# Optimization experiments

Hardware: AMD Instinct MI355X
Metric: run time of the kernel (lower is better)

## Reference

```python
import jax, jax.numpy as jnp
import numpy as np

B, S = 8, 1024                      # num sequences, per-seq prefill length (uniform ragged batch)
NUM_HEADS, HEAD_DIM, NUM_KV_HEADS = 32, 128, 8
GROUP = NUM_HEADS // NUM_KV_HEADS   # GQA repeat factor
SCALE = 1.0 / float(np.sqrt(HEAD_DIM))
T = B * S                           # total tokens in batch
NUM_SLOTS = 16384                   # KV-cache slots
DKV = NUM_KV_HEADS * HEAD_DIM


def setup_inputs() -> dict:
    key = jax.random.key(0)
    ks = jax.random.split(key, 4)
    q = jax.random.normal(ks[0], (T, NUM_HEADS * HEAD_DIM), dtype=jnp.float32)
    k = jax.random.normal(ks[1], (T, DKV), dtype=jnp.float32)
    v = jax.random.normal(ks[2], (T, DKV), dtype=jnp.float32)
    k_cache = jnp.zeros((NUM_SLOTS, DKV), dtype=jnp.float32)
    v_cache = jnp.zeros((NUM_SLOTS, DKV), dtype=jnp.float32)
    # distinct slots per token (pure prefill: gather mapping == store mapping)
    slot_mapping = jax.random.permutation(ks[3], NUM_SLOTS)[:T].astype(jnp.int32)
    seq_slot_mapping = slot_mapping
    return {"q": q, "k": k, "v": v, "k_cache": k_cache, "v_cache": v_cache,
            "slot_mapping": slot_mapping, "seq_slot_mapping": seq_slot_mapping}


def reference(q, k, v, k_cache, v_cache, slot_mapping, seq_slot_mapping):
    # reshape to per-head layout
    kr = k.reshape(T, DKV)
    vr = v.reshape(T, DKV)
    # store_kvcache: scatter new k/v into paged cache by slot
    k_cache = k_cache.at[slot_mapping].set(kr)
    v_cache = v_cache.at[slot_mapping].set(vr)
    # get_kvcache: gather the per-sequence contiguous KV from the cache
    ck = k_cache[seq_slot_mapping].reshape(B, S, NUM_KV_HEADS, HEAD_DIM)
    cv = v_cache[seq_slot_mapping].reshape(B, S, NUM_KV_HEADS, HEAD_DIM)
    qb = q.reshape(B, S, NUM_HEADS, HEAD_DIM)
    # GQA: repeat_interleave kv heads (matches torch SDPA enable_gqa)
    ck = jnp.repeat(ck, GROUP, axis=2)  # [B,S,H,D]
    cv = jnp.repeat(cv, GROUP, axis=2)
    scores = jnp.einsum("bqhd,bkhd->bhqk", qb, ck) * SCALE  # [B,H,S,S]
    causal = jnp.tril(jnp.ones((S, S), dtype=bool))
    scores = jnp.where(causal[None, None], scores, jnp.finfo(scores.dtype).min)
    probs = jax.nn.softmax(scores, axis=-1)
    o = jnp.einsum("bhqk,bkhd->bqhd", probs, cv)  # [B,S,H,D]
    return o.reshape(T, NUM_HEADS * HEAD_DIM)
```

## Files before the change

### kernel.cpp

```cpp
#include <hip/hip_runtime.h>

#define NB 8
#define NS 1024
#define NH 32
#define NKV 8
#define ND 128
#define QT 256
#define KT 64

typedef _Float16 f16x8 __attribute__((ext_vector_type(8)));
typedef __fp16 fp16x2 __attribute__((ext_vector_type(2)));
typedef float f32x16 __attribute__((ext_vector_type(16)));
typedef unsigned int u32x2 __attribute__((ext_vector_type(2)));

__device__ __forceinline__ float exp2fast(float x) { return __builtin_amdgcn_exp2f(x); }
__device__ __forceinline__ unsigned pkrtz_u(float a, float b) {
  union { fp16x2 h; unsigned u; } c;
  c.h = __builtin_amdgcn_cvt_pkrtz(a, b);
  return c.u;
}
__device__ __forceinline__ u32x2 swap32(float x) {
  union { float f; unsigned u; } c; c.f = x;
  return __builtin_amdgcn_permlane32_swap(c.u, c.u, false, false);
}
__device__ __forceinline__ float asf(unsigned u) { union { unsigned u; float f; } c; c.u = u; return c.f; }

__global__ __launch_bounds__(256)
void cvt_kf(const float* __restrict__ kg, char* __restrict__ wsK)
{
  int g = blockIdx.x * 256 + threadIdx.x;
  int t = g >> 7, c8 = g & 127;
  int hkv = c8 >> 4, d8 = c8 & 15;
  const float* src = kg + (size_t)t * 1024 + hkv * 128 + d8 * 8;
  float4 a = *(const float4*)src;
  float4 c = *(const float4*)(src + 4);
  f16x8 h8;
  h8[0] = (_Float16)a.x; h8[1] = (_Float16)a.y; h8[2] = (_Float16)a.z; h8[3] = (_Float16)a.w;
  h8[4] = (_Float16)c.x; h8[5] = (_Float16)c.y; h8[6] = (_Float16)c.z; h8[7] = (_Float16)c.w;
  int b  = t >> 10, kv = t & 1023;
  int ti = kv >> 6, kvl = kv & 63, kb = kvl >> 5, lq = kvl & 31;
  int dblk = d8 >> 1, hi = d8 & 1;
  size_t off = (((size_t)(b * 8 + hkv) * 16 + ti) * 16 + kb * 8 + dblk) * 1024 + (hi * 32 + lq) * 16;
  *(f16x8*)(wsK + off) = h8;
}

__global__ __launch_bounds__(256)
void cvt_vf(const float* __restrict__ vg, _Float16* __restrict__ wsV)
{
  __shared__ _Float16 T[ND][KT];
  const int tid = threadIdx.x;
  const int kvt = blockIdx.x, b = blockIdx.y, hkv = blockIdx.z;
#pragma unroll
  for (int pass = 0; pass < 8; ++pass) {
    int kvr = (tid >> 5) + pass * 8;
    int d4  = (tid & 31) * 4;
    float4 v = ((const float4*)vg)[(size_t)(b * NS + kvt * KT + kvr) * 256 + hkv * 32 + (tid & 31)];
    T[d4 + 0][kvr] = (_Float16)v.x;
    T[d4 + 1][kvr] = (_Float16)v.y;
    T[d4 + 2][kvr] = (_Float16)v.z;
    T[d4 + 3][kvr] = (_Float16)v.w;
  }
  __syncthreads();
  _Float16* out = wsV + ((size_t)(b * 8 + hkv) * 16 + kvt) * 8192;
#pragma unroll
  for (int pass = 0; pass < 4; ++pass) {
    int unit = tid + pass * 256;
    int c = unit >> 6, lane = unit & 63;
    int d = (c & 3) * 32 + (lane & 31);
    int kv8 = (c >> 2) * 16 + (lane >> 5) * 8;
    *(f16x8*)(out + unit * 8) = *(const f16x8*)&T[d][kv8];
  }
}

__global__ __launch_bounds__(512, 1)
void attn_fwd(const float* __restrict__ qg, const char* __restrict__ wsK,
              const char* __restrict__ wsV, float* __restrict__ og)
{
  __shared__ __align__(16) char Klds[2][16384];
  __shared__ __align__(16) char Vlds[2][16384];

  const int id = blockIdx.x;
  const int v  = (id & 7) * 32 + (id >> 3);
  const int panel = v >> 2;
  const int sub   = v & 3;
  const int b     = panel >> 3;
  const int hkv   = panel & 7;
  const int h     = hkv * 4 + sub;

  const int tid  = threadIdx.x;
  const int lane = tid & 63;
  const int w    = tid >> 6;
  const int lq   = lane & 31;
  const int hi   = lane >> 5;

  const float QS = 0.08838834764831845f * 1.4426950408889634f;

  const char* wsKb = wsK + (size_t)panel * 16 * 16384;
  const char* wsVb = wsV + (size_t)panel * 16 * 16384;

  const int o0 = tid * 16;
  const int o1 = (tid + 512) * 16;

  f16x8 kpre0, kpre1, vpre0, vpre1;

  const int qorder[4] = {0, 3, 1, 2};

#pragma unroll 1
  for (int ph = 0; ph < 4; ++ph) {
    const int qtile = qorder[ph];
    const int wv    = (ph & 1) ? (7 - w) : w;
    const int qr0w  = qtile * QT + wv * 32;
    const int qrow  = qr0w + lq;

    f16x8 qf[8];
    {
      const float* qp = qg + (size_t)(b * NS + qrow) * (NH * ND) + h * ND + hi * 8;
#pragma unroll
      for (int dblk = 0; dblk < 8; ++dblk) {
        float4 f0 = *(const float4*)(qp + dblk * 16);
        float4 f1 = *(const float4*)(qp + dblk * 16 + 4);
        f16x8 a;
        a[0] = (_Float16)(f0.x * QS); a[1] = (_Float16)(f0.y * QS);
        a[2] = (_Float16)(f0.z * QS); a[3] = (_Float16)(f0.w * QS);
        a[4] = (_Float16)(f1.x * QS); a[5] = (_Float16)(f1.y * QS);
        a[6] = (_Float16)(f1.z * QS); a[7] = (_Float16)(f1.w * QS);
        qf[dblk] = a;
      }
    }

    f32x16 acc[4];
#pragma unroll
    for (int nb = 0; nb < 4; ++nb)
#pragma unroll
      for (int r = 0; r < 16; ++r) acc[nb][r] = 0.f;
    float m_run = -1e30f, l_run = 0.f;

    const int nt = (qtile + 1) * (QT / KT);

    {
      kpre0 = *(const f16x8*)(wsKb + o0); kpre1 = *(const f16x8*)(wsKb + o1);
      vpre0 = *(const f16x8*)(wsVb + o0); vpre1 = *(const f16x8*)(wsVb + o1);
      *(f16x8*)(&Klds[0][0] + o0) = kpre0; *(f16x8*)(&Klds[0][0] + o1) = kpre1;
      *(f16x8*)(&Vlds[0][0] + o0) = vpre0; *(f16x8*)(&Vlds[0][0] + o1) = vpre1;
    }
    asm volatile("s_waitcnt lgkmcnt(0)" ::: "memory");
    __builtin_amdgcn_s_barrier();
    __builtin_amdgcn_sched_barrier(0);

#pragma unroll 1
    for (int ti = 0; ti < nt; ++ti) {
      const int kv0 = ti * KT;
      const int cur = ti & 1;
      const bool hn = (ti + 1 < nt);

      if (hn) {
        const char* gk = wsKb + (size_t)(ti + 1) * 16384;
        const char* gv = wsVb + (size_t)(ti + 1) * 16384;
        kpre0 = *(const f16x8*)(gk + o0); kpre1 = *(const f16x8*)(gk + o1);
        vpre0 = *(const f16x8*)(gv + o0); vpre1 = *(const f16x8*)(gv + o1);
      }

      const bool live = (kv0 <= qr0w + 31);
      f16x8 pa[4];
      if (live) {
        const char* Kb = &Klds[cur][0];

        f32x16 s[2];
#pragma unroll
        for (int r = 0; r < 16; ++r) { s[0][r] = 0.f; s[1][r] = 0.f; }
        __builtin_amdgcn_s_setprio(1);
#pragma unroll
        for (int dblk = 0; dblk < 8; ++dblk) {
          f16x8 k0 = *(const f16x8*)(Kb + dblk * 1024 + lane * 16);
          f16x8 k1 = *(const f16x8*)(Kb + (8 + dblk) * 1024 + lane * 16);
          s[0] = __builtin_amdgcn_mfma_f32_32x32x16_f16(k0, qf[dblk], s[0], 0, 0, 0);
          s[1] = __builtin_amdgcn_mfma_f32_32x32x16_f16(k1, qf[dblk], s[1], 0, 0, 0);
        }
        __builtin_amdgcn_s_setprio(0);

        if (kv0 + KT - 1 > qr0w) {
          const int thr = qrow - kv0;
#pragma unroll
          for (int kb = 0; kb < 2; ++kb)
#pragma unroll
            for (int r = 0; r < 16; ++r) {
              int kvl = kb * 32 + (r & 3) + 8 * (r >> 2) + 4 * hi;
              if (kvl > thr) s[kb][r] = -1e30f;
            }
        }

        float pmax = s[0][0];
#pragma unroll
        for (int r = 1; r < 16; ++r) pmax = fmaxf(pmax, s[0][r]);
#pragma unroll
        for (int r = 0; r < 16; ++r) pmax = fmaxf(pmax, s[1][r]);
        {
          u32x2 pr = swap32(pmax);
          pmax = fmaxf(asf(pr[0]), asf(pr[1]));
        }
        const int need = !__all(pmax <= m_run + 8.0f);
        if (need) {
          const float mn = fmaxf(m_run, pmax);
          const float al = exp2fast(m_run - mn);
          m_run = mn;
#pragma unroll
          for (int r = 0; r < 16; ++r) {
            int row = (r & 3) + 8 * (r >> 2) + 4 * hi;
            float a = __shfl(al, row, 64);
#pragma unroll
            for (int nb = 0; nb < 4; ++nb) acc[nb][r] *= a;
          }
          l_run *= al;
        }
        float rs = 0.f;
#pragma unroll
        for (int kb = 0; kb < 2; ++kb)
#pragma unroll
          for (int r = 0; r < 16; ++r) {
            float pv = exp2fast(s[kb][r] - m_run);
            s[kb][r] = pv;
            rs += pv;
          }
        {
          u32x2 sr = swap32(rs);
          rs = asf(sr[0]) + asf(sr[1]);
        }
        l_run += rs;

#pragma unroll
        for (int t = 0; t < 4; ++t) {
          const int kb = t >> 1, rb = (t & 1) * 8;
          unsigned w0 = pkrtz_u(s[kb][rb + 0], s[kb][rb + 1]);
          unsigned w1 = pkrtz_u(s[kb][rb + 2], s[kb][rb + 3]);
          unsigned w2 = pkrtz_u(s[kb][rb + 4], s[kb][rb + 5]);
          unsigned w3 = pkrtz_u(s[kb][rb + 6], s[kb][rb + 7]);
          u32x2 p02 = __builtin_amdgcn_permlane32_swap(w0, w2, false, false);
          u32x2 p13 = __builtin_amdgcn_permlane32_swap(w1, w3, false, false);
          union { unsigned u[4]; f16x8 v; } pw;
          pw.u[0] = p02[0]; pw.u[1] = p13[0]; pw.u[2] = p02[1]; pw.u[3] = p13[1];
          pa[t] = pw.v;
        }
      }

      if (hn) {
        *(f16x8*)(&Klds[cur ^ 1][0] + o0) = kpre0;
        *(f16x8*)(&Klds[cur ^ 1][0] + o1) = kpre1;
        *(f16x8*)(&Vlds[cur ^ 1][0] + o0) = vpre0;
        *(f16x8*)(&Vlds[cur ^ 1][0] + o1) = vpre1;
      }

      if (live) {
        const char* Vb = &Vlds[cur][0];
        __builtin_amdgcn_s_setprio(1);
#pragma unroll
        for (int t = 0; t < 4; ++t)
#pragma unroll
          for (int nb = 0; nb < 4; ++nb) {
            f16x8 vb = *(const f16x8*)(Vb + (t * 4 + nb) * 1024 + lane * 16);
            acc[nb] = __builtin_amdgcn_mfma_f32_32x32x16_f16(pa[t], vb, acc[nb], 0, 0, 0);
          }
        __builtin_amdgcn_s_setprio(0);
      }

      asm volatile("s_waitcnt lgkmcnt(0)" ::: "memory");
      __builtin_amdgcn_s_barrier();
      __builtin_amdgcn_sched_barrier(0);
    }

    const float linv = 1.0f / l_run;
#pragma unroll
    for (int r = 0; r < 16; ++r) {
      int row = (r & 3) + 8 * (r >> 2) + 4 * hi;
      float li = __shfl(linv, row, 64);
      float* op = og + (size_t)(b * NS + qr0w + row) * (NH * ND) + h * ND + lq;
#pragma unroll
      for (int nb = 0; nb < 4; ++nb)
        op[nb * 32] = acc[nb][r] * li;
    }
    __builtin_amdgcn_s_barrier();
  }
}

extern "C" void kernel_launch(void* const* d_in, const int* in_sizes, int n_in,
                              void* d_out, int out_size, void* d_ws, size_t ws_size,
                              hipStream_t stream) {
  const float* q = (const float*)d_in[0];
  const float* k = (const float*)d_in[1];
  const float* v = (const float*)d_in[2];
  float* o = (float*)d_out;

  const size_t KSZ = (size_t)NB * NKV * NS * ND * sizeof(_Float16);
  if (ws_size < 2 * KSZ) return;
  char*     wsK = (char*)d_ws;
  _Float16* wsV = (_Float16*)((char*)d_ws + KSZ);

  cvt_kf<<<dim3((NB * NS * 128) / 256), 256, 0, stream>>>(k, wsK);
  cvt_vf<<<dim3(NS / KT, NB, NKV),      256, 0, stream>>>(v, wsV);
  attn_fwd<<<dim3(256),                 512, 0, stream>>>(q, wsK, (const char*)wsV, o);
}
```

Baseline: 162.0 us.

## Process KV tiles in pairs with 4-stage LDS ring and staggered wave order

Expands the K/V LDS buffers from double to quad buffering and processes two KV tiles per loop iteration with a single barrier, halving barrier count. Odd and even waves process the two tiles in swapped order to desynchronize LDS reads and MFMA/softmax phases across waves. Global prefetch for the next pair is interleaved between the two tile computations. This costs twice the LDS footprint and more register pressure for the inlined lambda bodies.

```diff
diff --git a/kernel.cpp b/kernel.cpp
--- a/kernel.cpp
+++ b/kernel.cpp
@@ -76,8 +76,8 @@
 void attn_fwd(const float* __restrict__ qg, const char* __restrict__ wsK,
               const char* __restrict__ wsV, float* __restrict__ og)
 {
-  __shared__ __align__(16) char Klds[2][16384];
-  __shared__ __align__(16) char Vlds[2][16384];
+  __shared__ __align__(16) char Klds[4][16384];
+  __shared__ __align__(16) char Vlds[4][16384];
 
   const int id = blockIdx.x;
   const int v  = (id & 7) * 32 + (id >> 3);
@@ -135,131 +135,148 @@
       for (int r = 0; r < 16; ++r) acc[nb][r] = 0.f;
     float m_run = -1e30f, l_run = 0.f;
 
-    const int nt = (qtile + 1) * (QT / KT);
-
-    {
-      kpre0 = *(const f16x8*)(wsKb + o0); kpre1 = *(const f16x8*)(wsKb + o1);
-      vpre0 = *(const f16x8*)(wsVb + o0); vpre1 = *(const f16x8*)(wsVb + o1);
-      *(f16x8*)(&Klds[0][0] + o0) = kpre0; *(f16x8*)(&Klds[0][0] + o1) = kpre1;
-      *(f16x8*)(&Vlds[0][0] + o0) = vpre0; *(f16x8*)(&Vlds[0][0] + o1) = vpre1;
-    }
+    auto compute_tile = [&](int t) {
+      const int kv0 = t * KT;
+      if (kv0 > qr0w + 31) return;
+      const char* Kb = &Klds[t & 3][0];
+      const char* Vb = &Vlds[t & 3][0];
+
+      f32x16 s[2];
+#pragma unroll
+      for (int r = 0; r < 16; ++r) { s[0][r] = 0.f; s[1][r] = 0.f; }
+      __builtin_amdgcn_s_setprio(1);
+#pragma unroll
+      for (int dblk = 0; dblk < 8; ++dblk) {
+        f16x8 k0 = *(const f16x8*)(Kb + dblk * 1024 + lane * 16);
+        f16x8 k1 = *(const f16x8*)(Kb + (8 + dblk) * 1024 + lane * 16);
+        s[0] = __builtin_amdgcn_mfma_f32_32x32x16_f16(k0, qf[dblk], s[0], 0, 0, 0);
+        s[1] = __builtin_amdgcn_mfma_f32_32x32x16_f16(k1, qf[dblk], s[1], 0, 0, 0);
+      }
+      __builtin_amdgcn_s_setprio(0);
+
+      if (kv0 + KT - 1 > qr0w) {
+        const int thr = qrow - kv0;
+#pragma unroll
+        for (int kb = 0; kb < 2; ++kb)
+#pragma unroll
+          for (int r = 0; r < 16; ++r) {
+            int kvl = kb * 32 + (r & 3) + 8 * (r >> 2) + 4 * hi;
+            if (kvl > thr) s[kb][r] = -1e30f;
+          }
+      }
+
+      float pmax = s[0][0];
+#pragma unroll
+      for (int r = 1; r < 16; ++r) pmax = fmaxf(pmax, s[0][r]);
+#pragma unroll
+      for (int r = 0; r < 16; ++r) pmax = fmaxf(pmax, s[1][r]);
+      {
+        u32x2 pr = swap32(pmax);
+        pmax = fmaxf(asf(pr[0]), asf(pr[1]));
+      }
+      const int need = !__all(pmax <= m_run + 8.0f);
+      if (need) {
+        const float mn = fmaxf(m_run, pmax);
+        const float al = exp2fast(m_run - mn);
+        m_run = mn;
+#pragma unroll
+        for (int r = 0; r < 16; ++r) {
+          int row = (r & 3) + 8 * (r >> 2) + 4 * hi;
+          float a = __shfl(al, row, 64);
+#pragma unroll
+          for (int nb = 0; nb < 4; ++nb) acc[nb][r] *= a;
+        }
+        l_run *= al;
+      }
+      float rs = 0.f;
+#pragma unroll
+      for (int kb = 0; kb < 2; ++kb)
+#pragma unroll
+        for (int r = 0; r < 16; ++r) {
+          float pv = exp2fast(s[kb][r] - m_run);
+          s[kb][r] = pv;
+          rs += pv;
+        }
+      {
+        u32x2 sr = swap32(rs);
+        rs = asf(sr[0]) + asf(sr[1]);
+      }
+      l_run += rs;
+
+      f16x8 pa[4];
+#pragma unroll
+      for (int t4 = 0; t4 < 4; ++t4) {
+        const int kb = t4 >> 1, rb = (t4 & 1) * 8;
+        unsigned w0 = pkrtz_u(s[kb][rb + 0], s[kb][rb + 1]);
+        unsigned w1 = pkrtz_u(s[kb][rb + 2], s[kb][rb + 3]);
+        unsigned w2 = pkrtz_u(s[kb][rb + 4], s[kb][rb + 5]);
+        unsigned w3 = pkrtz_u(s[kb][rb + 6], s[kb][rb + 7]);
+        u32x2 p02 = __builtin_amdgcn_permlane32_swap(w0, w2, false, false);
+        u32x2 p13 = __builtin_amdgcn_permlane32_swap(w1, w3, false, false);
+        union { unsigned u[4]; f16x8 v; } pw;
+        pw.u[0] = p02[0]; pw.u[1] = p13[0]; pw.u[2] = p02[1]; pw.u[3] = p13[1];
+        pa[t4] = pw.v;
+      }
+
+      __builtin_amdgcn_s_setprio(1);
+#pragma unroll
+      for (int t4 = 0; t4 < 4; ++t4)
+#pragma unroll
+        for (int nb = 0; nb < 4; ++nb) {
+          f16x8 vb = *(const f16x8*)(Vb + (t4 * 4 + nb) * 1024 + lane * 16);
+          acc[nb] = __builtin_amdgcn_mfma_f32_32x32x16_f16(pa[t4], vb, acc[nb], 0, 0, 0);
+        }
+      __builtin_amdgcn_s_setprio(0);
+    };
+
+    const int npairs = 2 * (qtile + 1);
+
+    kpre0 = *(const f16x8*)(wsKb + o0); kpre1 = *(const f16x8*)(wsKb + o1);
+    vpre0 = *(const f16x8*)(wsVb + o0); vpre1 = *(const f16x8*)(wsVb + o1);
+    *(f16x8*)(&Klds[0][0] + o0) = kpre0; *(f16x8*)(&Klds[0][0] + o1) = kpre1;
+    *(f16x8*)(&Vlds[0][0] + o0) = vpre0; *(f16x8*)(&Vlds[0][0] + o1) = vpre1;
+    kpre0 = *(const f16x8*)(wsKb + 16384 + o0); kpre1 = *(const f16x8*)(wsKb + 16384 + o1);
+    vpre0 = *(const f16x8*)(wsVb + 16384 + o0); vpre1 = *(const f16x8*)(wsVb + 16384 + o1);
+    *(f16x8*)(&Klds[1][0] + o0) = kpre0; *(f16x8*)(&Klds[1][0] + o1) = kpre1;
+    *(f16x8*)(&Vlds[1][0] + o0) = vpre0; *(f16x8*)(&Vlds[1][0] + o1) = vpre1;
     asm volatile("s_waitcnt lgkmcnt(0)" ::: "memory");
     __builtin_amdgcn_s_barrier();
     __builtin_amdgcn_sched_barrier(0);
 
 #pragma unroll 1
-    for (int ti = 0; ti < nt; ++ti) {
-      const int kv0 = ti * KT;
-      const int cur = ti & 1;
-      const bool hn = (ti + 1 < nt);
+    for (int pj = 0; pj < npairs; ++pj) {
+      const int a  = 2 * pj;
+      const bool hn = (pj + 1 < npairs);
+      const int t1 = (w & 1) ? a + 1 : a;
+      const int t2 = (w & 1) ? a : a + 1;
 
       if (hn) {
-        const char* gk = wsKb + (size_t)(ti + 1) * 16384;
-        const char* gv = wsVb + (size_t)(ti + 1) * 16384;
+        const char* gk = wsKb + (size_t)(a + 2) * 16384;
+        const char* gv = wsVb + (size_t)(a + 2) * 16384;
         kpre0 = *(const f16x8*)(gk + o0); kpre1 = *(const f16x8*)(gk + o1);
         vpre0 = *(const f16x8*)(gv + o0); vpre1 = *(const f16x8*)(gv + o1);
       }
 
-      const bool live = (kv0 <= qr0w + 31);
-      f16x8 pa[4];
-      if (live) {
-        const char* Kb = &Klds[cur][0];
-
-        f32x16 s[2];
-#pragma unroll
-        for (int r = 0; r < 16; ++r) { s[0][r] = 0.f; s[1][r] = 0.f; }
-        __builtin_amdgcn_s_setprio(1);
-#pragma unroll
-        for (int dblk = 0; dblk < 8; ++dblk) {
-          f16x8 k0 = *(const f16x8*)(Kb + dblk * 1024 + lane * 16);
-          f16x8 k1 = *(const f16x8*)(Kb + (8 + dblk) * 1024 + lane * 16);
-          s[0] = __builtin_amdgcn_mfma_f32_32x32x16_f16(k0, qf[dblk], s[0], 0, 0, 0);
-          s[1] = __builtin_amdgcn_mfma_f32_32x32x16_f16(k1, qf[dblk], s[1], 0, 0, 0);
-        }
-        __builtin_amdgcn_s_setprio(0);
-
-        if (kv0 + KT - 1 > qr0w) {
-          const int thr = qrow - kv0;
-#pragma unroll
-          for (int kb = 0; kb < 2; ++kb)
-#pragma unroll
-            for (int r = 0; r < 16; ++r) {
-              int kvl = kb * 32 + (r & 3) + 8 * (r >> 2) + 4 * hi;
-              if (kvl > thr) s[kb][r] = -1e30f;
-            }
-        }
-
-        float pmax = s[0][0];
-#pragma unroll
-        for (int r = 1; r < 16; ++r) pmax = fmaxf(pmax, s[0][r]);
-#pragma unroll
-        for (int r = 0; r < 16; ++r) pmax = fmaxf(pmax, s[1][r]);
-        {
-          u32x2 pr = swap32(pmax);
-          pmax = fmaxf(asf(pr[0]), asf(pr[1]));
-        }
-        const int need = !__all(pmax <= m_run + 8.0f);
-        if (need) {
-          const float mn = fmaxf(m_run, pmax);
-          const float al = exp2fast(m_run - mn);
-          m_run = mn;
-#pragma unroll
-          for (int r = 0; r < 16; ++r) {
-            int row = (r & 3) + 8 * (r >> 2) + 4 * hi;
-            float a = __shfl(al, row, 64);
-#pragma unroll
-            for (int nb = 0; nb < 4; ++nb) acc[nb][r] *= a;
-          }
-          l_run *= al;
-        }
-        float rs = 0.f;
-#pragma unroll
-        for (int kb = 0; kb < 2; ++kb)
-#pragma unroll
-          for (int r = 0; r < 16; ++r) {
-            float pv = exp2fast(s[kb][r] - m_run);
-            s[kb][r] = pv;
-            rs += pv;
-          }
-        {
-          u32x2 sr = swap32(rs);
-          rs = asf(sr[0]) + asf(sr[1]);
-        }
-        l_run += rs;
-
-#pragma unroll
-        for (int t = 0; t < 4; ++t) {
-          const int kb = t >> 1, rb = (t & 1) * 8;
-          unsigned w0 = pkrtz_u(s[kb][rb + 0], s[kb][rb + 1]);
-          unsigned w1 = pkrtz_u(s[kb][rb + 2], s[kb][rb + 3]);
-          unsigned w2 = pkrtz_u(s[kb][rb + 4], s[kb][rb + 5]);
-          unsigned w3 = pkrtz_u(s[kb][rb + 6], s[kb][rb + 7]);
-          u32x2 p02 = __builtin_amdgcn_permlane32_swap(w0, w2, false, false);
-          u32x2 p13 = __builtin_amdgcn_permlane32_swap(w1, w3, false, false);
-          union { unsigned u[4]; f16x8 v; } pw;
-          pw.u[0] = p02[0]; pw.u[1] = p13[0]; pw.u[2] = p02[1]; pw.u[3] = p13[1];
-          pa[t] = pw.v;
-        }
-      }
+      compute_tile(t1);
 
       if (hn) {
-        *(f16x8*)(&Klds[cur ^ 1][0] + o0) = kpre0;
-        *(f16x8*)(&Klds[cur ^ 1][0] + o1) = kpre1;
-        *(f16x8*)(&Vlds[cur ^ 1][0] + o0) = vpre0;
-        *(f16x8*)(&Vlds[cur ^ 1][0] + o1) = vpre1;
-      }
-
-      if (live) {
-        const char* Vb = &Vlds[cur][0];
-        __builtin_amdgcn_s_setprio(1);
-#pragma unroll
-        for (int t = 0; t < 4; ++t)
-#pragma unroll
-          for (int nb = 0; nb < 4; ++nb) {
-            f16x8 vb = *(const f16x8*)(Vb + (t * 4 + nb) * 1024 + lane * 16);
-            acc[nb] = __builtin_amdgcn_mfma_f32_32x32x16_f16(pa[t], vb, acc[nb], 0, 0, 0);
-          }
-        __builtin_amdgcn_s_setprio(0);
+        *(f16x8*)(&Klds[(a + 2) & 3][0] + o0) = kpre0;
+        *(f16x8*)(&Klds[(a + 2) & 3][0] + o1) = kpre1;
+        *(f16x8*)(&Vlds[(a + 2) & 3][0] + o0) = vpre0;
+        *(f16x8*)(&Vlds[(a + 2) & 3][0] + o1) = vpre1;
+        const char* gk = wsKb + (size_t)(a + 3) * 16384;
+        const char* gv = wsVb + (size_t)(a + 3) * 16384;
+        kpre0 = *(const f16x8*)(gk + o0); kpre1 = *(const f16x8*)(gk + o1);
+        vpre0 = *(const f16x8*)(gv + o0); vpre1 = *(const f16x8*)(gv + o1);
+      }
+
+      compute_tile(t2);
+
+      if (hn) {
+        *(f16x8*)(&Klds[(a + 3) & 3][0] + o0) = kpre0;
+        *(f16x8*)(&Klds[(a + 3) & 3][0] + o1) = kpre1;
+        *(f16x8*)(&Vlds[(a + 3) & 3][0] + o0) = vpre0;
+        *(f16x8*)(&Vlds[(a + 3) & 3][0] + o1) = vpre1;
       }
 
       asm volatile("s_waitcnt lgkmcnt(0)" ::: "memory");
```

Result: faster. 157.7 us, median of 3 (-2.7%).

## Switch attention to 16x16x32 MFMA tiles with LDS-staged P and smaller query tiles

Applied to the files above, without the earlier changes.

Replaces the 32x32x16 MFMA layout with 16x16x32 MFMAs, so each wave now owns 16 query rows and each block handles 128-row query tiles over eight phases. The K and V workspace layouts are rewritten to match the new fragment shapes. The P matrix is routed through a swizzled per-wave LDS buffer instead of permlane swaps. Launch bounds now allow higher occupancy, aiming to cut register pressure and improve causal load balance, at the cost of extra LDS traffic and more K/V tile reloads per block.

```diff
diff --git a/kernel.cpp b/kernel.cpp
--- a/kernel.cpp
+++ b/kernel.cpp
@@ -5,13 +5,11 @@
 #define NH 32
 #define NKV 8
 #define ND 128
-#define QT 256
 #define KT 64
 
 typedef _Float16 f16x8 __attribute__((ext_vector_type(8)));
 typedef __fp16 fp16x2 __attribute__((ext_vector_type(2)));
-typedef float f32x16 __attribute__((ext_vector_type(16)));
-typedef unsigned int u32x2 __attribute__((ext_vector_type(2)));
+typedef float f32x4v __attribute__((ext_vector_type(4)));
 
 __device__ __forceinline__ float exp2fast(float x) { return __builtin_amdgcn_exp2f(x); }
 __device__ __forceinline__ unsigned pkrtz_u(float a, float b) {
@@ -19,11 +17,6 @@
   c.h = __builtin_amdgcn_cvt_pkrtz(a, b);
   return c.u;
 }
-__device__ __forceinline__ u32x2 swap32(float x) {
-  union { float f; unsigned u; } c; c.f = x;
-  return __builtin_amdgcn_permlane32_swap(c.u, c.u, false, false);
-}
-__device__ __forceinline__ float asf(unsigned u) { union { unsigned u; float f; } c; c.u = u; return c.f; }
 
 __global__ __launch_bounds__(256)
 void cvt_kf(const float* __restrict__ kg, char* __restrict__ wsK)
@@ -38,9 +31,9 @@
   h8[0] = (_Float16)a.x; h8[1] = (_Float16)a.y; h8[2] = (_Float16)a.z; h8[3] = (_Float16)a.w;
   h8[4] = (_Float16)c.x; h8[5] = (_Float16)c.y; h8[6] = (_Float16)c.z; h8[7] = (_Float16)c.w;
   int b  = t >> 10, kv = t & 1023;
-  int ti = kv >> 6, kvl = kv & 63, kb = kvl >> 5, lq = kvl & 31;
-  int dblk = d8 >> 1, hi = d8 & 1;
-  size_t off = (((size_t)(b * 8 + hkv) * 16 + ti) * 16 + kb * 8 + dblk) * 1024 + (hi * 32 + lq) * 16;
+  int ti = kv >> 6, kvl = kv & 63, st = kvl >> 4, r = kvl & 15;
+  int dblk = d8 >> 2, lg = d8 & 3;
+  size_t off = (((size_t)(b * 8 + hkv) * 16 + ti) * 16 + (st * 4 + dblk)) * 1024 + (lg * 16 + r) * 16;
   *(f16x8*)(wsK + off) = h8;
 }
 
@@ -66,18 +59,19 @@
   for (int pass = 0; pass < 4; ++pass) {
     int unit = tid + pass * 256;
     int c = unit >> 6, lane = unit & 63;
-    int d = (c & 3) * 32 + (lane & 31);
-    int kv8 = (c >> 2) * 16 + (lane >> 5) * 8;
-    *(f16x8*)(out + unit * 8) = *(const f16x8*)&T[d][kv8];
+    int m = c >> 3, nb = c & 7;
+    int r = lane & 15, lg = lane >> 4;
+    *(f16x8*)(out + unit * 8) = *(const f16x8*)&T[16 * nb + r][32 * m + 8 * lg];
   }
 }
 
-__global__ __launch_bounds__(512, 1)
+__global__ __launch_bounds__(512, 4)
 void attn_fwd(const float* __restrict__ qg, const char* __restrict__ wsK,
               const char* __restrict__ wsV, float* __restrict__ og)
 {
   __shared__ __align__(16) char Klds[2][16384];
   __shared__ __align__(16) char Vlds[2][16384];
+  __shared__ __align__(16) char Plds[8][2048];
 
   const int id = blockIdx.x;
   const int v  = (id & 7) * 32 + (id >> 3);
@@ -90,8 +84,8 @@
   const int tid  = threadIdx.x;
   const int lane = tid & 63;
   const int w    = tid >> 6;
-  const int lq   = lane & 31;
-  const int hi   = lane >> 5;
+  const int r    = lane & 15;
+  const int lg   = lane >> 4;
 
   const float QS = 0.08838834764831845f * 1.4426950408889634f;
 
@@ -103,22 +97,23 @@
 
   f16x8 kpre0, kpre1, vpre0, vpre1;
 
-  const int qorder[4] = {0, 3, 1, 2};
+  char* Pw = &Plds[w][0];
+  const int psw = (r & 7) << 4;
 
 #pragma unroll 1
-  for (int ph = 0; ph < 4; ++ph) {
-    const int qtile = qorder[ph];
+  for (int ph = 0; ph < 8; ++ph) {
+    const int qtile = (ph & 1) ? (7 - (ph >> 1)) : (ph >> 1);
     const int wv    = (ph & 1) ? (7 - w) : w;
-    const int qr0w  = qtile * QT + wv * 32;
-    const int qrow  = qr0w + lq;
-
-    f16x8 qf[8];
+    const int qr0w  = qtile * 128 + wv * 16;
+    const int qrow  = qr0w + r;
+
+    f16x8 qf[4];
     {
-      const float* qp = qg + (size_t)(b * NS + qrow) * (NH * ND) + h * ND + hi * 8;
-#pragma unroll
-      for (int dblk = 0; dblk < 8; ++dblk) {
-        float4 f0 = *(const float4*)(qp + dblk * 16);
-        float4 f1 = *(const float4*)(qp + dblk * 16 + 4);
+      const float* qp = qg + (size_t)(b * NS + qrow) * (NH * ND) + h * ND + lg * 8;
+#pragma unroll
+      for (int dblk = 0; dblk < 4; ++dblk) {
+        float4 f0 = *(const float4*)(qp + dblk * 32);
+        float4 f1 = *(const float4*)(qp + dblk * 32 + 4);
         f16x8 a;
         a[0] = (_Float16)(f0.x * QS); a[1] = (_Float16)(f0.y * QS);
         a[2] = (_Float16)(f0.z * QS); a[3] = (_Float16)(f0.w * QS);
@@ -128,21 +123,19 @@
       }
     }
 
-    f32x16 acc[4];
-#pragma unroll
-    for (int nb = 0; nb < 4; ++nb)
-#pragma unroll
-      for (int r = 0; r < 16; ++r) acc[nb][r] = 0.f;
+    f32x4v acc[8];
+#pragma unroll
+    for (int nb = 0; nb < 8; ++nb)
+#pragma unroll
+      for (int j = 0; j < 4; ++j) acc[nb][j] = 0.f;
     float m_run = -1e30f, l_run = 0.f;
 
-    const int nt = (qtile + 1) * (QT / KT);
-
-    {
-      kpre0 = *(const f16x8*)(wsKb + o0); kpre1 = *(const f16x8*)(wsKb + o1);
-      vpre0 = *(const f16x8*)(wsVb + o0); vpre1 = *(const f16x8*)(wsVb + o1);
-      *(f16x8*)(&Klds[0][0] + o0) = kpre0; *(f16x8*)(&Klds[0][0] + o1) = kpre1;
-      *(f16x8*)(&Vlds[0][0] + o0) = vpre0; *(f16x8*)(&Vlds[0][0] + o1) = vpre1;
-    }
+    const int nt = 2 * (qtile + 1);
+
+    kpre0 = *(const f16x8*)(wsKb + o0); kpre1 = *(const f16x8*)(wsKb + o1);
+    vpre0 = *(const f16x8*)(wsVb + o0); vpre1 = *(const f16x8*)(wsVb + o1);
+    *(f16x8*)(&Klds[0][0] + o0) = kpre0; *(f16x8*)(&Klds[0][0] + o1) = kpre1;
+    *(f16x8*)(&Vlds[0][0] + o0) = vpre0; *(f16x8*)(&Vlds[0][0] + o1) = vpre1;
     asm volatile("s_waitcnt lgkmcnt(0)" ::: "memory");
     __builtin_amdgcn_s_barrier();
     __builtin_amdgcn_sched_barrier(0);
@@ -160,86 +153,89 @@
         vpre0 = *(const f16x8*)(gv + o0); vpre1 = *(const f16x8*)(gv + o1);
       }
 
-      const bool live = (kv0 <= qr0w + 31);
-      f16x8 pa[4];
+      const bool live = (kv0 <= qr0w + 15);
       if (live) {
         const char* Kb = &Klds[cur][0];
 
-        f32x16 s[2];
-#pragma unroll
-        for (int r = 0; r < 16; ++r) { s[0][r] = 0.f; s[1][r] = 0.f; }
+        f32x4v s[4];
+#pragma unroll
+        for (int st = 0; st < 4; ++st)
+#pragma unroll
+          for (int j = 0; j < 4; ++j) s[st][j] = 0.f;
         __builtin_amdgcn_s_setprio(1);
 #pragma unroll
-        for (int dblk = 0; dblk < 8; ++dblk) {
-          f16x8 k0 = *(const f16x8*)(Kb + dblk * 1024 + lane * 16);
-          f16x8 k1 = *(const f16x8*)(Kb + (8 + dblk) * 1024 + lane * 16);
-          s[0] = __builtin_amdgcn_mfma_f32_32x32x16_f16(k0, qf[dblk], s[0], 0, 0, 0);
-          s[1] = __builtin_amdgcn_mfma_f32_32x32x16_f16(k1, qf[dblk], s[1], 0, 0, 0);
-        }
+        for (int dblk = 0; dblk < 4; ++dblk)
+#pragma unroll
+          for (int st = 0; st < 4; ++st) {
+            f16x8 kf = *(const f16x8*)(Kb + (st * 4 + dblk) * 1024 + lane * 16);
+            s[st] = __builtin_amdgcn_mfma_f32_16x16x32_f16(kf, qf[dblk], s[st], 0, 0, 0);
+          }
         __builtin_amdgcn_s_setprio(0);
 
         if (kv0 + KT - 1 > qr0w) {
           const int thr = qrow - kv0;
 #pragma unroll
-          for (int kb = 0; kb < 2; ++kb)
-#pragma unroll
-            for (int r = 0; r < 16; ++r) {
-              int kvl = kb * 32 + (r & 3) + 8 * (r >> 2) + 4 * hi;
-              if (kvl > thr) s[kb][r] = -1e30f;
-            }
+          for (int st = 0; st < 4; ++st)
+#pragma unroll
+            for (int j = 0; j < 4; ++j)
+              if (16 * st + 4 * lg + j > thr) s[st][j] = -1e30f;
         }
 
-        float pmax = s[0][0];
-#pragma unroll
-        for (int r = 1; r < 16; ++r) pmax = fmaxf(pmax, s[0][r]);
-#pragma unroll
-        for (int r = 0; r < 16; ++r) pmax = fmaxf(pmax, s[1][r]);
-        {
-          u32x2 pr = swap32(pmax);
-          pmax = fmaxf(asf(pr[0]), asf(pr[1]));
-        }
+        float tm[4];
+#pragma unroll
+        for (int st = 0; st < 4; ++st)
+          tm[st] = fmaxf(fmaxf(s[st][0], s[st][1]), fmaxf(s[st][2], s[st][3]));
+        float pmax = fmaxf(fmaxf(tm[0], tm[1]), fmaxf(tm[2], tm[3]));
+        pmax = fmaxf(pmax, __shfl_xor(pmax, 16));
+        pmax = fmaxf(pmax, __shfl_xor(pmax, 32));
         const int need = !__all(pmax <= m_run + 8.0f);
         if (need) {
           const float mn = fmaxf(m_run, pmax);
           const float al = exp2fast(m_run - mn);
           m_run = mn;
 #pragma unroll
-          for (int r = 0; r < 16; ++r) {
-            int row = (r & 3) + 8 * (r >> 2) + 4 * hi;
-            float a = __shfl(al, row, 64);
-#pragma unroll
-            for (int nb = 0; nb < 4; ++nb) acc[nb][r] *= a;
+          for (int j = 0; j < 4; ++j) {
+            float a = __shfl(al, 4 * lg + j, 64);
+#pragma unroll
+            for (int nb = 0; nb < 8; ++nb) acc[nb][j] *= a;
           }
           l_run *= al;
         }
-        float rs = 0.f;
-#pragma unroll
-        for (int kb = 0; kb < 2; ++kb)
-#pragma unroll
-          for (int r = 0; r < 16; ++r) {
-            float pv = exp2fast(s[kb][r] - m_run);
-            s[kb][r] = pv;
-            rs += pv;
-          }
-        {
-          u32x2 sr = swap32(rs);
-          rs = asf(sr[0]) + asf(sr[1]);
+#pragma unroll
+        for (int st = 0; st < 4; ++st)
+#pragma unroll
+          for (int j = 0; j < 4; ++j)
+            s[st][j] = exp2fast(s[st][j] - m_run);
+        float ts[4];
+#pragma unroll
+        for (int st = 0; st < 4; ++st)
+          ts[st] = (s[st][0] + s[st][1]) + (s[st][2] + s[st][3]);
+        float rs = (ts[0] + ts[1]) + (ts[2] + ts[3]);
+        rs += __shfl_xor(rs, 16);
+        rs += __shfl_xor(rs, 32);
+        l_run += rs;
+
+#pragma unroll
+        for (int st = 0; st < 4; ++st)
+#pragma unroll
+          for (int j2 = 0; j2 < 2; ++j2) {
+            unsigned u = pkrtz_u(s[st][2 * j2], s[st][2 * j2 + 1]);
+            int kvb = (16 * st + 4 * lg + 2 * j2) * 2;
+            *(unsigned*)(Pw + r * 128 + (kvb ^ psw)) = u;
+          }
+
+        const char* Vb = &Vlds[cur][0];
+        __builtin_amdgcn_s_setprio(1);
+#pragma unroll
+        for (int m = 0; m < 2; ++m) {
+          f16x8 pa = *(const f16x8*)(Pw + r * 128 + ((64 * m + 16 * lg) ^ psw));
+#pragma unroll
+          for (int nb = 0; nb < 8; ++nb) {
+            f16x8 vb = *(const f16x8*)(Vb + (m * 8 + nb) * 1024 + lane * 16);
+            acc[nb] = __builtin_amdgcn_mfma_f32_16x16x32_f16(pa, vb, acc[nb], 0, 0, 0);
+          }
         }
-        l_run += rs;
-
-#pragma unroll
-        for (int t = 0; t < 4; ++t) {
-          const int kb = t >> 1, rb = (t & 1) * 8;
-          unsigned w0 = pkrtz_u(s[kb][rb + 0], s[kb][rb + 1]);
-          unsigned w1 = pkrtz_u(s[kb][rb + 2], s[kb][rb + 3]);
-          unsigned w2 = pkrtz_u(s[kb][rb + 4], s[kb][rb + 5]);
-          unsigned w3 = pkrtz_u(s[kb][rb + 6], s[kb][rb + 7]);
-          u32x2 p02 = __builtin_amdgcn_permlane32_swap(w0, w2, false, false);
-          u32x2 p13 = __builtin_amdgcn_permlane32_swap(w1, w3, false, false);
-          union { unsigned u[4]; f16x8 v; } pw;
-          pw.u[0] = p02[0]; pw.u[1] = p13[0]; pw.u[2] = p02[1]; pw.u[3] = p13[1];
-          pa[t] = pw.v;
-        }
+        __builtin_amdgcn_s_setprio(0);
       }
 
       if (hn) {
@@ -249,19 +245,6 @@
         *(f16x8*)(&Vlds[cur ^ 1][0] + o1) = vpre1;
       }
 
-      if (live) {
-        const char* Vb = &Vlds[cur][0];
-        __builtin_amdgcn_s_setprio(1);
-#pragma unroll
-        for (int t = 0; t < 4; ++t)
-#pragma unroll
-          for (int nb = 0; nb < 4; ++nb) {
-            f16x8 vb = *(const f16x8*)(Vb + (t * 4 + nb) * 1024 + lane * 16);
-            acc[nb] = __builtin_amdgcn_mfma_f32_32x32x16_f16(pa[t], vb, acc[nb], 0, 0, 0);
-          }
-        __builtin_amdgcn_s_setprio(0);
-      }
-
       asm volatile("s_waitcnt lgkmcnt(0)" ::: "memory");
       __builtin_amdgcn_s_barrier();
       __builtin_amdgcn_sched_barrier(0);
@@ -269,13 +252,13 @@
 
     const float linv = 1.0f / l_run;
 #pragma unroll
-    for (int r = 0; r < 16; ++r) {
-      int row = (r & 3) + 8 * (r >> 2) + 4 * hi;
-      float li = __shfl(linv, row, 64);
-      float* op = og + (size_t)(b * NS + qr0w + row) * (NH * ND) + h * ND + lq;
-#pragma unroll
-      for (int nb = 0; nb < 4; ++nb)
-        op[nb * 32] = acc[nb][r] * li;
+    for (int j = 0; j < 4; ++j) {
+      float li = __shfl(linv, 4 * lg + j, 64);
+      const int row = qr0w + 4 * lg + j;
+      float* op = og + (size_t)(b * NS + row) * (NH * ND) + h * ND + r;
+#pragma unroll
+      for (int nb = 0; nb < 8; ++nb)
+        op[nb * 16] = acc[nb][j] * li;
     }
     __builtin_amdgcn_s_barrier();
   }
```

Result: slower. 209.3 us (+29.2%).
